# Optimization experiments

Hardware: AMD Instinct MI355X
Metric: run time of the kernel (lower is better)

The kernel has to match this reference:

```python
import jax, jax.numpy as jnp
import numpy as np

U = 256   # units
D = 256   # input_dim
B = 65536 # batch


def hard_tanh(x):
    return jnp.clip(x, -1.0, 1.0)


def binarize(x):
    # sign quantization (forward); straight-through in the bwd module
    return jnp.where(x >= 0, 1.0, -1.0).astype(x.dtype)


def setup_inputs() -> dict:
    key = jax.random.key(0)
    k1, k2, k3, k4, k5 = jax.random.split(key, 5)
    return {
        "inputs": jax.random.normal(k1, (B, D), dtype=jnp.float32),
        "h": jax.random.normal(k2, (B, U), dtype=jnp.float32),
        "c": jax.random.normal(k3, (B, U), dtype=jnp.float32),
        "kernel": jax.random.normal(k4, (D, 4 * U), dtype=jnp.float32) * 0.05,
        "recurrent_kernel": jax.random.normal(k5, (U, 4 * U), dtype=jnp.float32) * 0.05,
    }


def reference(inputs, h, c, kernel, recurrent_kernel):
    u = kernel.shape[1] // 4
    h_tm1 = hard_tanh(h)
    c_tm1 = hard_tanh(c)
    # binarized input projection, hard_tanh applied to each gate pre-activation
    x_all = hard_tanh(inputs @ binarize(kernel))            # [B, 4U]
    x_i, x_f, x_c, x_o = (x_all[:, :u], x_all[:, u:2*u],
                          x_all[:, 2*u:3*u], x_all[:, 3*u:])
    # binarized recurrent projection
    r_all = h_tm1 @ binarize(recurrent_kernel)              # [B, 4U]
    r_i, r_f, r_c, r_o = (r_all[:, :u], r_all[:, u:2*u],
                          r_all[:, 2*u:3*u], r_all[:, 3*u:])
    # NOTE: faithful to source: f pairs x_i with W_f, i pairs x_f with W_i
    f = hard_tanh(x_i + r_f)
    i = hard_tanh(x_f + r_i)
    c_new = f * c_tm1 + i * hard_tanh(x_c + r_c)
    o = hard_tanh(x_o + r_o)
    h_new = hard_tanh(o * hard_tanh(c_new))
    return (h_new, h_new, c_new)
```

## Files before the change

### kernel.cpp

```cpp
#include <hip/hip_runtime.h>


#define NB 65536

typedef _Float16 f16x8 __attribute__((ext_vector_type(8)));
typedef float f32x16 __attribute__((ext_vector_type(16)));

__device__ __forceinline__ float htanh(float x) { return fminf(1.f, fmaxf(-1.f, x)); }

__global__ void prep_w(const float* __restrict__ Kf, const float* __restrict__ RKf,
                       unsigned short* __restrict__ wfrag) {
  __shared__ unsigned short sgn[32][72];
  const int b = blockIdx.x;
  const int side = b >> 7, kt = (b >> 4) & 7, nt = b & 15;
  const float* M = side ? RKf : Kf;
  const int t = threadIdx.x;

  {
    const int k = t >> 3, n8 = (t & 7) << 3;
    const float* p = M + (kt * 32 + k) * 1024 + nt * 64 + n8;
    float4 v0 = *(const float4*)p;
    float4 v1 = *(const float4*)(p + 4);
    float xs[8] = {v0.x, v0.y, v0.z, v0.w, v1.x, v1.y, v1.z, v1.w};
#pragma unroll
    for (int i = 0; i < 8; ++i)
      sgn[k][n8 + i] = (xs[i] >= 0.f) ? 0x3C00u : 0xBC00u;
  }
  __syncthreads();

  const int fl = t >> 6, l = t & 63;
  const int j = fl >> 1, uhh = fl & 1;
  const int nloc = uhh * 32 + (l & 31);
  const int kloc = j * 16 + (l >> 5) * 8;
  unsigned short o[8];
#pragma unroll
  for (int e = 0; e < 8; ++e) o[e] = sgn[kloc + e][nloc];
  const int ng = nt * 64 + nloc;
  const int gate = ng >> 8, u32 = (ng >> 5) & 7;
  const int k16 = kt * 2 + j;
  const int fragid = ((k16 * 2 + side) * 8 + u32) * 4 + gate;
  uint4 ov;
  ov.x = (unsigned)o[0] | ((unsigned)o[1] << 16);
  ov.y = (unsigned)o[2] | ((unsigned)o[3] << 16);
  ov.z = (unsigned)o[4] | ((unsigned)o[5] << 16);
  ov.w = (unsigned)o[6] | ((unsigned)o[7] << 16);
  *(uint4*)((char*)wfrag + fragid * 1024 + l * 16) = ov;
}

__global__ __launch_bounds__(256, 4)
void blstm_main(const float* __restrict__ xin, const float* __restrict__ hin,
                const float* __restrict__ cin, const unsigned short* __restrict__ wfrag,
                float* __restrict__ out) {
  __shared__ char smem[32768];

  const int bid = blockIdx.x;
  const int swz = (bid & 7) * 1024 + (bid >> 3);
  const int m0 = (swz >> 2) << 5;
  const int ub = swz & 3;

  const int tid = threadIdx.x;
  const int lane = tid & 63;
  const int w = tid >> 6;
  const int wu = w & 1, sw = w >> 1;
  const int l31 = lane & 31, lh = lane >> 5;

  const int sSide = tid >> 7;
  const int sRow = (tid & 127) >> 2;
  const int sQ = tid & 3;
  const float* aPtr = (sSide ? hin : xin) + (m0 + sRow) * 256 + sQ * 8;
  char* const aWr = smem + sSide * 4224 + sQ * 528 + sRow * 16;
  const char* const aRd = smem + sw * 4224 + lh * 528 + l31 * 16;

  const unsigned short* const wq = wfrag + ((sw * 8 + ub * 2 + wu) << 11) + lane * 8;

  f32x16 acc[4] = {};
  f16x8 wf[4];
  f16x8 ah, al;
  float4 a0 = *(const float4*)(aPtr);
  float4 a1 = *(const float4*)(aPtr + 4);

#define MFMA4(AF) do {                                                      \
    acc[0] = __builtin_amdgcn_mfma_f32_32x32x16_f16(AF, wf[0], acc[0], 0, 0, 0); \
    acc[1] = __builtin_amdgcn_mfma_f32_32x32x16_f16(AF, wf[1], acc[1], 0, 0, 0); \
    acc[2] = __builtin_amdgcn_mfma_f32_32x32x16_f16(AF, wf[2], acc[2], 0, 0, 0); \
    acc[3] = __builtin_amdgcn_mfma_f32_32x32x16_f16(AF, wf[3], acc[3], 0, 0, 0); \
  } while (0)

#define STEP(S) do {                                                        \
          \
    {                                                                       \
      float xs_[8] = {a0.x, a0.y, a0.z, a0.w, a1.x, a1.y, a1.z, a1.w};      \
      f16x8 hv_, lv_;                                                       \
      _Pragma("unroll")                                                     \
      for (int i_ = 0; i_ < 8; ++i_) {                                      \
        float x_ = xs_[i_];                                                 \
        if (sSide) x_ = htanh(x_);                                          \
        _Float16 hf_ = (_Float16)x_;                                        \
        hv_[i_] = hf_;                                                      \
        lv_[i_] = (_Float16)(x_ - (float)hf_);                              \
      }                                                                     \
      char* wr_ = aWr + ((S) & 1) * 8448;                                   \
      *(f16x8*)(wr_) = hv_;                                                 \
      *(f16x8*)(wr_ + 2112) = lv_;                                          \
    }                                                                       \
    if ((S) < 7) {                                                          \
      a0 = *(const float4*)(aPtr + ((S) + 1) * 32);                         \
      a1 = *(const float4*)(aPtr + ((S) + 1) * 32 + 4);                     \
    }                                                                       \
                 \
    {                                                                       \
      const unsigned short* wp_ = wq + ((S) * 2) * 32768;                   \
      wf[0] = *(const f16x8*)(wp_);                                         \
      wf[1] = *(const f16x8*)(wp_ + 512);                                   \
      wf[2] = *(const f16x8*)(wp_ + 1024);                                  \
      wf[3] = *(const f16x8*)(wp_ + 1536);                                  \
    }                                                                       \
    asm volatile("s_waitcnt lgkmcnt(0)\n\ts_barrier" ::: "memory");         \
    {                                                                       \
      const char* rd_ = aRd + ((S) & 1) * 8448;                             \
      ah = *(const f16x8*)(rd_);                                \
      al = *(const f16x8*)(rd_ + 2112);                         \
      MFMA4(ah);                                                            \
      MFMA4(al);                                                            \
                 \
      const unsigned short* wp_ = wq + ((S) * 2 + 1) * 32768;               \
      wf[0] = *(const f16x8*)(wp_);                                         \
      wf[1] = *(const f16x8*)(wp_ + 512);                                   \
      wf[2] = *(const f16x8*)(wp_ + 1024);                                  \
      wf[3] = *(const f16x8*)(wp_ + 1536);                                  \
      ah = *(const f16x8*)(rd_ + 1056);                         \
      al = *(const f16x8*)(rd_ + 2112 + 1056);                  \
      MFMA4(ah);                                                            \
      MFMA4(al);                                                            \
    }                                                                       \
  } while (0)

  STEP(0); STEP(1); STEP(2); STEP(3);
  STEP(4); STEP(5); STEP(6); STEP(7);
#undef STEP
#undef MFMA4

  __syncthreads();
  float* ex = (float*)(smem + wu * 16384);

  if (sw == 1) {
#pragma unroll
    for (int g = 0; g < 4; ++g)
#pragma unroll
      for (int q = 0; q < 4; ++q) {
        float4 v;
        v.x = acc[g][q * 4 + 0]; v.y = acc[g][q * 4 + 1];
        v.z = acc[g][q * 4 + 2]; v.w = acc[g][q * 4 + 3];
        *(float4*)((char*)ex + (g * 4 + q) * 1024 + lane * 16) = v;
      }
  }
  __syncthreads();
  if (sw == 0) {
    const int gu = ub * 64 + wu * 32 + l31;
#pragma unroll
    for (int q = 0; q < 4; ++q) {
      float4 ri = *(const float4*)((const char*)ex + (0 * 4 + q) * 1024 + lane * 16);
      float4 rf = *(const float4*)((const char*)ex + (1 * 4 + q) * 1024 + lane * 16);
      float4 rc = *(const float4*)((const char*)ex + (2 * 4 + q) * 1024 + lane * 16);
      float4 ro = *(const float4*)((const char*)ex + (3 * 4 + q) * 1024 + lane * 16);
#pragma unroll
      for (int t = 0; t < 4; ++t) {
        const int r = q * 4 + t;
        const int row = t + q * 8 + lh * 4;
        const int grow = m0 + row;
        const float xi = htanh(acc[0][r]);
        const float xf = htanh(acc[1][r]);
        const float xc = htanh(acc[2][r]);
        const float xo = htanh(acc[3][r]);
        const float riv = ((const float*)&ri)[t];
        const float rfv = ((const float*)&rf)[t];
        const float rcv = ((const float*)&rc)[t];
        const float rov = ((const float*)&ro)[t];
        const float fg   = htanh(xi + rfv);
        const float ig   = htanh(xf + riv);
        const float cand = htanh(xc + rcv);
        const float og   = htanh(xo + rov);
        const float ct = htanh(cin[grow * 256 + gu]);
        const float cn = fg * ct + ig * cand;
        const float hn = htanh(og * htanh(cn));
        const int o1 = grow * 256 + gu;
        out[o1] = hn;
        out[NB * 256 + o1] = hn;
        out[2 * NB * 256 + o1] = cn;
      }
    }
  }
}

extern "C" void kernel_launch(void* const* d_in, const int* in_sizes, int n_in,
                              void* d_out, int out_size, void* d_ws, size_t ws_size,
                              hipStream_t stream) {
  const float* xin = (const float*)d_in[0];
  const float* hin = (const float*)d_in[1];
  const float* cin = (const float*)d_in[2];
  const float* kf  = (const float*)d_in[3];
  const float* rkf = (const float*)d_in[4];
  float* out = (float*)d_out;

  unsigned short* wfrag = (unsigned short*)d_ws;

  prep_w<<<256, 256, 0, stream>>>(kf, rkf, wfrag);
  blstm_main<<<8192, 256, 0, stream>>>(xin, hin, cin, wfrag, out);
}
```

Before: 199.2 us.

## Software-pipeline K loop with prefetch, staggered K order, and packed conversions

Restructures the main K loop so that LDS fragments and weight fragments for the next half-step are loaded before the MFMAs, and the next A tile is converted and written to LDS while the current one is consumed. A per-block phase rotates the starting K slice so blocks read different weight slices at the same time. It also uses packed RTZ fp16 conversion, fmed3 for clamping, and s_setprio around the MFMAs, and lowers the occupancy hint from 4 to 3 blocks per CU. These changes trade register pressure and occupancy for latency hiding, and RTZ rounding slightly changes the hi/lo fp16 split.

```diff
diff --git a/kernel.cpp b/kernel.cpp
--- a/kernel.cpp
+++ b/kernel.cpp
@@ -4,9 +4,12 @@
 #define NB 65536
 
 typedef _Float16 f16x8 __attribute__((ext_vector_type(8)));
+typedef __fp16 fp16x2 __attribute__((ext_vector_type(2)));
 typedef float f32x16 __attribute__((ext_vector_type(16)));
 
-__device__ __forceinline__ float htanh(float x) { return fminf(1.f, fmaxf(-1.f, x)); }
+__device__ __forceinline__ float htanh(float x) {
+  return __builtin_amdgcn_fmed3f(x, -1.0f, 1.0f);
+}
 
 __global__ void prep_w(const float* __restrict__ Kf, const float* __restrict__ RKf,
                        unsigned short* __restrict__ wfrag) {
@@ -47,7 +50,7 @@
   *(uint4*)((char*)wfrag + fragid * 1024 + l * 16) = ov;
 }
 
-__global__ __launch_bounds__(256, 4)
+__global__ __launch_bounds__(256, 3)
 void blstm_main(const float* __restrict__ xin, const float* __restrict__ hin,
                 const float* __restrict__ cin, const unsigned short* __restrict__ wfrag,
                 float* __restrict__ out) {
@@ -57,6 +60,7 @@
   const int swz = (bid & 7) * 1024 + (bid >> 3);
   const int m0 = (swz >> 2) << 5;
   const int ub = swz & 3;
+  const int phase = (bid >> 3) & 7;
 
   const int tid = threadIdx.x;
   const int lane = tid & 63;
@@ -71,74 +75,100 @@
   char* const aWr = smem + sSide * 4224 + sQ * 528 + sRow * 16;
   const char* const aRd = smem + sw * 4224 + lh * 528 + l31 * 16;
 
-  const unsigned short* const wq = wfrag + ((sw * 8 + ub * 2 + wu) << 11) + lane * 8;
+  const char* const wqB = (const char*)wfrag + ((sw * 8 + ub * 2 + wu) << 12) + lane * 16;
 
   f32x16 acc[4] = {};
-  f16x8 wf[4];
-  f16x8 ah, al;
-  float4 a0 = *(const float4*)(aPtr);
-  float4 a1 = *(const float4*)(aPtr + 4);
-
-#define MFMA4(AF) do {                                                      \
-    acc[0] = __builtin_amdgcn_mfma_f32_32x32x16_f16(AF, wf[0], acc[0], 0, 0, 0); \
-    acc[1] = __builtin_amdgcn_mfma_f32_32x32x16_f16(AF, wf[1], acc[1], 0, 0, 0); \
-    acc[2] = __builtin_amdgcn_mfma_f32_32x32x16_f16(AF, wf[2], acc[2], 0, 0, 0); \
-    acc[3] = __builtin_amdgcn_mfma_f32_32x32x16_f16(AF, wf[3], acc[3], 0, 0, 0); \
+  f16x8 wa0, wa1, wa2, wa3;
+  float4 a0, a1;
+
+#define CONVERT_WRITE(WRBUF) do {                                           \
+    float x0_ = a0.x, x1_ = a0.y, x2_ = a0.z, x3_ = a0.w;                   \
+    float x4_ = a1.x, x5_ = a1.y, x6_ = a1.z, x7_ = a1.w;                   \
+    if (sSide) {                                                            \
+      x0_ = htanh(x0_); x1_ = htanh(x1_); x2_ = htanh(x2_); x3_ = htanh(x3_); \
+      x4_ = htanh(x4_); x5_ = htanh(x5_); x6_ = htanh(x6_); x7_ = htanh(x7_); \
+    }                                                                       \
+    fp16x2 h01_ = __builtin_amdgcn_cvt_pkrtz(x0_, x1_);                     \
+    fp16x2 h23_ = __builtin_amdgcn_cvt_pkrtz(x2_, x3_);                     \
+    fp16x2 h45_ = __builtin_amdgcn_cvt_pkrtz(x4_, x5_);                     \
+    fp16x2 h67_ = __builtin_amdgcn_cvt_pkrtz(x6_, x7_);                     \
+    fp16x2 l01_ = __builtin_amdgcn_cvt_pkrtz(x0_ - (float)h01_[0], x1_ - (float)h01_[1]); \
+    fp16x2 l23_ = __builtin_amdgcn_cvt_pkrtz(x2_ - (float)h23_[0], x3_ - (float)h23_[1]); \
+    fp16x2 l45_ = __builtin_amdgcn_cvt_pkrtz(x4_ - (float)h45_[0], x5_ - (float)h45_[1]); \
+    fp16x2 l67_ = __builtin_amdgcn_cvt_pkrtz(x6_ - (float)h67_[0], x7_ - (float)h67_[1]); \
+    uint4 H_, L_;                                                           \
+    H_.x = __builtin_bit_cast(unsigned, h01_); H_.y = __builtin_bit_cast(unsigned, h23_); \
+    H_.z = __builtin_bit_cast(unsigned, h45_); H_.w = __builtin_bit_cast(unsigned, h67_); \
+    L_.x = __builtin_bit_cast(unsigned, l01_); L_.y = __builtin_bit_cast(unsigned, l23_); \
+    L_.z = __builtin_bit_cast(unsigned, l45_); L_.w = __builtin_bit_cast(unsigned, l67_); \
+    *(uint4*)(WRBUF) = H_;                                                  \
+    *(uint4*)((WRBUF) + 2112) = L_;                                         \
   } while (0)
 
+#define MFMA4(AF, W0, W1, W2, W3) do {                                      \
+    acc[0] = __builtin_amdgcn_mfma_f32_32x32x16_f16(AF, W0, acc[0], 0, 0, 0); \
+    acc[1] = __builtin_amdgcn_mfma_f32_32x32x16_f16(AF, W1, acc[1], 0, 0, 0); \
+    acc[2] = __builtin_amdgcn_mfma_f32_32x32x16_f16(AF, W2, acc[2], 0, 0, 0); \
+    acc[3] = __builtin_amdgcn_mfma_f32_32x32x16_f16(AF, W3, acc[3], 0, 0, 0); \
+  } while (0)
+
+  {
+    const int s0 = phase;
+    a0 = *(const float4*)(aPtr + s0 * 32);
+    a1 = *(const float4*)(aPtr + s0 * 32 + 4);
+    const char* wp0 = wqB + s0 * 131072;
+    wa0 = *(const f16x8*)(wp0);
+    wa1 = *(const f16x8*)(wp0 + 1024);
+    wa2 = *(const f16x8*)(wp0 + 2048);
+    wa3 = *(const f16x8*)(wp0 + 3072);
+    CONVERT_WRITE(aWr);
+    const int s1 = (phase + 1) & 7;
+    a0 = *(const float4*)(aPtr + s1 * 32);
+    a1 = *(const float4*)(aPtr + s1 * 32 + 4);
+    asm volatile("s_waitcnt lgkmcnt(0)\n\ts_barrier" ::: "memory");
+  }
+
 #define STEP(S) do {                                                        \
-          \
-    {                                                                       \
-      float xs_[8] = {a0.x, a0.y, a0.z, a0.w, a1.x, a1.y, a1.z, a1.w};      \
-      f16x8 hv_, lv_;                                                       \
-      _Pragma("unroll")                                                     \
-      for (int i_ = 0; i_ < 8; ++i_) {                                      \
-        float x_ = xs_[i_];                                                 \
-        if (sSide) x_ = htanh(x_);                                          \
-        _Float16 hf_ = (_Float16)x_;                                        \
-        hv_[i_] = hf_;                                                      \
-        lv_[i_] = (_Float16)(x_ - (float)hf_);                              \
-      }                                                                     \
-      char* wr_ = aWr + ((S) & 1) * 8448;                                   \
-      *(f16x8*)(wr_) = hv_;                                                 \
-      *(f16x8*)(wr_ + 2112) = lv_;                                          \
+    const int s_ = ((S) + phase) & 7;                                       \
+    const char* rd_ = aRd + ((S) & 1) * 8448;                               \
+    f16x8 ah0_ = *(const f16x8*)(rd_);                                      \
+    f16x8 al0_ = *(const f16x8*)(rd_ + 2112);                               \
+    f16x8 ah1_ = *(const f16x8*)(rd_ + 1056);                               \
+    f16x8 al1_ = *(const f16x8*)(rd_ + 3168);                               \
+                     \
+    const char* wpB_ = wqB + s_ * 131072 + 65536;                           \
+    f16x8 wb0_ = *(const f16x8*)(wpB_);                                     \
+    f16x8 wb1_ = *(const f16x8*)(wpB_ + 1024);                              \
+    f16x8 wb2_ = *(const f16x8*)(wpB_ + 2048);                              \
+    f16x8 wb3_ = *(const f16x8*)(wpB_ + 3072);                              \
+     \
+    if ((S) < 7) CONVERT_WRITE(aWr + (((S) + 1) & 1) * 8448);               \
+    if ((S) < 6) {                                                          \
+      const int s2_ = ((S) + 2 + phase) & 7;                                \
+      a0 = *(const float4*)(aPtr + s2_ * 32);                               \
+      a1 = *(const float4*)(aPtr + s2_ * 32 + 4);                           \
     }                                                                       \
-    if ((S) < 7) {                                                          \
-      a0 = *(const float4*)(aPtr + ((S) + 1) * 32);                         \
-      a1 = *(const float4*)(aPtr + ((S) + 1) * 32 + 4);                     \
+    __builtin_amdgcn_s_setprio(1);                                          \
+    MFMA4(ah0_, wa0, wa1, wa2, wa3);                                        \
+    MFMA4(al0_, wa0, wa1, wa2, wa3);                                        \
+    if ((S) < 7) {      \
+      const char* wpN_ = wqB + ((((S) + 1 + phase) & 7)) * 131072;          \
+      wa0 = *(const f16x8*)(wpN_);                                          \
+      wa1 = *(const f16x8*)(wpN_ + 1024);                                   \
+      wa2 = *(const f16x8*)(wpN_ + 2048);                                   \
+      wa3 = *(const f16x8*)(wpN_ + 3072);                                   \
     }                                                                       \
-                 \
-    {                                                                       \
-      const unsigned short* wp_ = wq + ((S) * 2) * 32768;                   \
-      wf[0] = *(const f16x8*)(wp_);                                         \
-      wf[1] = *(const f16x8*)(wp_ + 512);                                   \
-      wf[2] = *(const f16x8*)(wp_ + 1024);                                  \
-      wf[3] = *(const f16x8*)(wp_ + 1536);                                  \
-    }                                                                       \
+    MFMA4(ah1_, wb0_, wb1_, wb2_, wb3_);                                    \
+    MFMA4(al1_, wb0_, wb1_, wb2_, wb3_);                                    \
+    __builtin_amdgcn_s_setprio(0);                                          \
     asm volatile("s_waitcnt lgkmcnt(0)\n\ts_barrier" ::: "memory");         \
-    {                                                                       \
-      const char* rd_ = aRd + ((S) & 1) * 8448;                             \
-      ah = *(const f16x8*)(rd_);                                \
-      al = *(const f16x8*)(rd_ + 2112);                         \
-      MFMA4(ah);                                                            \
-      MFMA4(al);                                                            \
-                 \
-      const unsigned short* wp_ = wq + ((S) * 2 + 1) * 32768;               \
-      wf[0] = *(const f16x8*)(wp_);                                         \
-      wf[1] = *(const f16x8*)(wp_ + 512);                                   \
-      wf[2] = *(const f16x8*)(wp_ + 1024);                                  \
-      wf[3] = *(const f16x8*)(wp_ + 1536);                                  \
-      ah = *(const f16x8*)(rd_ + 1056);                         \
-      al = *(const f16x8*)(rd_ + 2112 + 1056);                  \
-      MFMA4(ah);                                                            \
-      MFMA4(al);                                                            \
-    }                                                                       \
   } while (0)
 
   STEP(0); STEP(1); STEP(2); STEP(3);
   STEP(4); STEP(5); STEP(6); STEP(7);
 #undef STEP
 #undef MFMA4
+#undef CONVERT_WRITE
 
   __syncthreads();
   float* ex = (float*)(smem + wu * 16384);
```

After: 205.2 us. +3.0%, slower.

## Give each wave a private LDS staging buffer and drop per-step barriers

Applied to the files above, without the earlier changes.

Restructures the K loop so each wave converts and stages only its own 32-row A tile (hi/lo fp16 split) in a private double-buffered LDS region. This removes the block-wide s_barrier on every step, prefetches two steps ahead, and loads both halves of the weight fragments up front. It also switches to packed cvt_pkrtz conversions, uses fmed3 for hard-tanh, raises MFMA issue priority, and lowers launch bounds to 3 waves per SIMD. The costs are more registers, duplicated global loads (waves sharing a row band now each read the same A rows), and round-to-zero conversion, which changes the hi/lo split slightly.

```diff
diff --git a/kernel.cpp b/kernel.cpp
--- a/kernel.cpp
+++ b/kernel.cpp
@@ -4,9 +4,12 @@
 #define NB 65536
 
 typedef _Float16 f16x8 __attribute__((ext_vector_type(8)));
+typedef __fp16 fp16x2 __attribute__((ext_vector_type(2)));
 typedef float f32x16 __attribute__((ext_vector_type(16)));
 
-__device__ __forceinline__ float htanh(float x) { return fminf(1.f, fmaxf(-1.f, x)); }
+__device__ __forceinline__ float htanh(float x) {
+  return __builtin_amdgcn_fmed3f(x, -1.0f, 1.0f);
+}
 
 __global__ void prep_w(const float* __restrict__ Kf, const float* __restrict__ RKf,
                        unsigned short* __restrict__ wfrag) {
@@ -47,7 +50,7 @@
   *(uint4*)((char*)wfrag + fragid * 1024 + l * 16) = ov;
 }
 
-__global__ __launch_bounds__(256, 4)
+__global__ __launch_bounds__(256, 3)
 void blstm_main(const float* __restrict__ xin, const float* __restrict__ hin,
                 const float* __restrict__ cin, const unsigned short* __restrict__ wfrag,
                 float* __restrict__ out) {
@@ -64,81 +67,109 @@
   const int wu = w & 1, sw = w >> 1;
   const int l31 = lane & 31, lh = lane >> 5;
 
-  const int sSide = tid >> 7;
-  const int sRow = (tid & 127) >> 2;
-  const int sQ = tid & 3;
-  const float* aPtr = (sSide ? hin : xin) + (m0 + sRow) * 256 + sQ * 8;
-  char* const aWr = smem + sSide * 4224 + sQ * 528 + sRow * 16;
-  const char* const aRd = smem + sw * 4224 + lh * 528 + l31 * 16;
-
-  const unsigned short* const wq = wfrag + ((sw * 8 + ub * 2 + wu) << 11) + lane * 8;
+  char* const myBuf = smem + w * 8192;
+  char* const wrB = myBuf + (lh * 2) * 512 + l31 * 16;
+  const char* const rdB = myBuf + lh * 512 + l31 * 16;
+
+  const float* const aP = (sw ? hin : xin) + (m0 + l31) * 256 + lh * 16;
+
+  const char* const wqB = (const char*)wfrag + ((sw * 8 + ub * 2 + wu) << 12) + lane * 16;
 
   f32x16 acc[4] = {};
-  f16x8 wf[4];
-  f16x8 ah, al;
-  float4 a0 = *(const float4*)(aPtr);
-  float4 a1 = *(const float4*)(aPtr + 4);
-
-#define MFMA4(AF) do {                                                      \
-    acc[0] = __builtin_amdgcn_mfma_f32_32x32x16_f16(AF, wf[0], acc[0], 0, 0, 0); \
-    acc[1] = __builtin_amdgcn_mfma_f32_32x32x16_f16(AF, wf[1], acc[1], 0, 0, 0); \
-    acc[2] = __builtin_amdgcn_mfma_f32_32x32x16_f16(AF, wf[2], acc[2], 0, 0, 0); \
-    acc[3] = __builtin_amdgcn_mfma_f32_32x32x16_f16(AF, wf[3], acc[3], 0, 0, 0); \
+  float4 a0, a1, a2, a3;
+
+#define ALOAD(S) do {                                                       \
+    a0 = *(const float4*)(aP + (S) * 32);                                   \
+    a1 = *(const float4*)(aP + (S) * 32 + 4);                               \
+    a2 = *(const float4*)(aP + (S) * 32 + 8);                               \
+    a3 = *(const float4*)(aP + (S) * 32 + 12);                              \
   } while (0)
 
-#define STEP(S) do {                                                        \
-          \
-    {                                                                       \
-      float xs_[8] = {a0.x, a0.y, a0.z, a0.w, a1.x, a1.y, a1.z, a1.w};      \
-      f16x8 hv_, lv_;                                                       \
-      _Pragma("unroll")                                                     \
-      for (int i_ = 0; i_ < 8; ++i_) {                                      \
-        float x_ = xs_[i_];                                                 \
-        if (sSide) x_ = htanh(x_);                                          \
-        _Float16 hf_ = (_Float16)x_;                                        \
-        hv_[i_] = hf_;                                                      \
-        lv_[i_] = (_Float16)(x_ - (float)hf_);                              \
-      }                                                                     \
-      char* wr_ = aWr + ((S) & 1) * 8448;                                   \
-      *(f16x8*)(wr_) = hv_;                                                 \
-      *(f16x8*)(wr_ + 2112) = lv_;                                          \
+#define CW(DST) do {                                                        \
+    float v0_ = a0.x, v1_ = a0.y, v2_ = a0.z, v3_ = a0.w;                   \
+    float v4_ = a1.x, v5_ = a1.y, v6_ = a1.z, v7_ = a1.w;                   \
+    float v8_ = a2.x, v9_ = a2.y, vA_ = a2.z, vB_ = a2.w;                   \
+    float vC_ = a3.x, vD_ = a3.y, vE_ = a3.z, vF_ = a3.w;                   \
+    if (sw) {                                                               \
+      v0_ = htanh(v0_); v1_ = htanh(v1_); v2_ = htanh(v2_); v3_ = htanh(v3_); \
+      v4_ = htanh(v4_); v5_ = htanh(v5_); v6_ = htanh(v6_); v7_ = htanh(v7_); \
+      v8_ = htanh(v8_); v9_ = htanh(v9_); vA_ = htanh(vA_); vB_ = htanh(vB_); \
+      vC_ = htanh(vC_); vD_ = htanh(vD_); vE_ = htanh(vE_); vF_ = htanh(vF_); \
     }                                                                       \
-    if ((S) < 7) {                                                          \
-      a0 = *(const float4*)(aPtr + ((S) + 1) * 32);                         \
-      a1 = *(const float4*)(aPtr + ((S) + 1) * 32 + 4);                     \
-    }                                                                       \
-                 \
-    {                                                                       \
-      const unsigned short* wp_ = wq + ((S) * 2) * 32768;                   \
-      wf[0] = *(const f16x8*)(wp_);                                         \
-      wf[1] = *(const f16x8*)(wp_ + 512);                                   \
-      wf[2] = *(const f16x8*)(wp_ + 1024);                                  \
-      wf[3] = *(const f16x8*)(wp_ + 1536);                                  \
-    }                                                                       \
-    asm volatile("s_waitcnt lgkmcnt(0)\n\ts_barrier" ::: "memory");         \
-    {                                                                       \
-      const char* rd_ = aRd + ((S) & 1) * 8448;                             \
-      ah = *(const f16x8*)(rd_);                                \
-      al = *(const f16x8*)(rd_ + 2112);                         \
-      MFMA4(ah);                                                            \
-      MFMA4(al);                                                            \
-                 \
-      const unsigned short* wp_ = wq + ((S) * 2 + 1) * 32768;               \
-      wf[0] = *(const f16x8*)(wp_);                                         \
-      wf[1] = *(const f16x8*)(wp_ + 512);                                   \
-      wf[2] = *(const f16x8*)(wp_ + 1024);                                  \
-      wf[3] = *(const f16x8*)(wp_ + 1536);                                  \
-      ah = *(const f16x8*)(rd_ + 1056);                         \
-      al = *(const f16x8*)(rd_ + 2112 + 1056);                  \
-      MFMA4(ah);                                                            \
-      MFMA4(al);                                                            \
-    }                                                                       \
+    fp16x2 h01_ = __builtin_amdgcn_cvt_pkrtz(v0_, v1_);                     \
+    fp16x2 h23_ = __builtin_amdgcn_cvt_pkrtz(v2_, v3_);                     \
+    fp16x2 h45_ = __builtin_amdgcn_cvt_pkrtz(v4_, v5_);                     \
+    fp16x2 h67_ = __builtin_amdgcn_cvt_pkrtz(v6_, v7_);                     \
+    fp16x2 h89_ = __builtin_amdgcn_cvt_pkrtz(v8_, v9_);                     \
+    fp16x2 hAB_ = __builtin_amdgcn_cvt_pkrtz(vA_, vB_);                     \
+    fp16x2 hCD_ = __builtin_amdgcn_cvt_pkrtz(vC_, vD_);                     \
+    fp16x2 hEF_ = __builtin_amdgcn_cvt_pkrtz(vE_, vF_);                     \
+    fp16x2 l01_ = __builtin_amdgcn_cvt_pkrtz(v0_ - (float)h01_[0], v1_ - (float)h01_[1]); \
+    fp16x2 l23_ = __builtin_amdgcn_cvt_pkrtz(v2_ - (float)h23_[0], v3_ - (float)h23_[1]); \
+    fp16x2 l45_ = __builtin_amdgcn_cvt_pkrtz(v4_ - (float)h45_[0], v5_ - (float)h45_[1]); \
+    fp16x2 l67_ = __builtin_amdgcn_cvt_pkrtz(v6_ - (float)h67_[0], v7_ - (float)h67_[1]); \
+    fp16x2 l89_ = __builtin_amdgcn_cvt_pkrtz(v8_ - (float)h89_[0], v9_ - (float)h89_[1]); \
+    fp16x2 lAB_ = __builtin_amdgcn_cvt_pkrtz(vA_ - (float)hAB_[0], vB_ - (float)hAB_[1]); \
+    fp16x2 lCD_ = __builtin_amdgcn_cvt_pkrtz(vC_ - (float)hCD_[0], vD_ - (float)hCD_[1]); \
+    fp16x2 lEF_ = __builtin_amdgcn_cvt_pkrtz(vE_ - (float)hEF_[0], vF_ - (float)hEF_[1]); \
+    uint4 H0_, H1_, L0_, L1_;                                               \
+    H0_.x = __builtin_bit_cast(unsigned, h01_); H0_.y = __builtin_bit_cast(unsigned, h23_); \
+    H0_.z = __builtin_bit_cast(unsigned, h45_); H0_.w = __builtin_bit_cast(unsigned, h67_); \
+    H1_.x = __builtin_bit_cast(unsigned, h89_); H1_.y = __builtin_bit_cast(unsigned, hAB_); \
+    H1_.z = __builtin_bit_cast(unsigned, hCD_); H1_.w = __builtin_bit_cast(unsigned, hEF_); \
+    L0_.x = __builtin_bit_cast(unsigned, l01_); L0_.y = __builtin_bit_cast(unsigned, l23_); \
+    L0_.z = __builtin_bit_cast(unsigned, l45_); L0_.w = __builtin_bit_cast(unsigned, l67_); \
+    L1_.x = __builtin_bit_cast(unsigned, l89_); L1_.y = __builtin_bit_cast(unsigned, lAB_); \
+    L1_.z = __builtin_bit_cast(unsigned, lCD_); L1_.w = __builtin_bit_cast(unsigned, lEF_); \
+    *(uint4*)(DST) = H0_;                                                   \
+    *(uint4*)((DST) + 512) = H1_;                                           \
+    *(uint4*)((DST) + 2048) = L0_;                                          \
+    *(uint4*)((DST) + 2560) = L1_;                                          \
   } while (0)
 
-  STEP(0); STEP(1); STEP(2); STEP(3);
-  STEP(4); STEP(5); STEP(6); STEP(7);
-#undef STEP
+#define MFMA4(AF, W0, W1, W2, W3) do {                                      \
+    acc[0] = __builtin_amdgcn_mfma_f32_32x32x16_f16(AF, W0, acc[0], 0, 0, 0); \
+    acc[1] = __builtin_amdgcn_mfma_f32_32x32x16_f16(AF, W1, acc[1], 0, 0, 0); \
+    acc[2] = __builtin_amdgcn_mfma_f32_32x32x16_f16(AF, W2, acc[2], 0, 0, 0); \
+    acc[3] = __builtin_amdgcn_mfma_f32_32x32x16_f16(AF, W3, acc[3], 0, 0, 0); \
+  } while (0)
+
+  ALOAD(0);
+  CW(wrB);
+  ALOAD(1);
+
+#pragma unroll
+  for (int s = 0; s < 8; ++s) {
+    const char* rb = rdB + (s & 1) * 4096;
+    f16x8 ah0 = *(const f16x8*)(rb);
+    f16x8 ah1 = *(const f16x8*)(rb + 1024);
+    f16x8 al0 = *(const f16x8*)(rb + 2048);
+    f16x8 al1 = *(const f16x8*)(rb + 3072);
+
+    const char* wp0 = wqB + (s * 2) * 65536;
+    f16x8 wa0 = *(const f16x8*)(wp0);
+    f16x8 wa1 = *(const f16x8*)(wp0 + 1024);
+    f16x8 wa2 = *(const f16x8*)(wp0 + 2048);
+    f16x8 wa3 = *(const f16x8*)(wp0 + 3072);
+    const char* wp1 = wp0 + 65536;
+    f16x8 wb0 = *(const f16x8*)(wp1);
+    f16x8 wb1 = *(const f16x8*)(wp1 + 1024);
+    f16x8 wb2 = *(const f16x8*)(wp1 + 2048);
+    f16x8 wb3 = *(const f16x8*)(wp1 + 3072);
+
+    if (s < 7) CW(wrB + ((s + 1) & 1) * 4096);
+    if (s < 6) ALOAD(s + 2);
+
+    __builtin_amdgcn_s_setprio(1);
+    MFMA4(ah0, wa0, wa1, wa2, wa3);
+    MFMA4(al0, wa0, wa1, wa2, wa3);
+    MFMA4(ah1, wb0, wb1, wb2, wb3);
+    MFMA4(al1, wb0, wb1, wb2, wb3);
+    __builtin_amdgcn_s_setprio(0);
+  }
 #undef MFMA4
+#undef CW
+#undef ALOAD
 
   __syncthreads();
   float* ex = (float*)(smem + wu * 16384);
```

Measured after the change: 255.7 us. +28.4%, slower.
